# Kernel optimization log

Measured on AMD Instinct MI355X. Metric: run time of the kernel, lower is better.

Reference implementation:

```python
import jax, jax.numpy as jnp
import numpy as np

B, P, H, D = 32, 512, 512, 512

def setup_inputs() -> dict:
    key = jax.random.key(0)
    k1, k2, k3, k4 = jax.random.split(key, 4)
    px = jax.random.normal(k1, (B, P, D), dtype=jnp.float32)
    hx = jax.random.normal(k2, (B, H, D), dtype=jnp.float32)
    p_mask = jax.random.randint(k3, (B, P), 0, 2) == 1  # True = padded
    h_mask = jax.random.randint(k4, (B, H), 0, 2) == 1
    return {"px": px, "hx": hx, "p_mask": p_mask, "h_mask": h_mask}

def reference(px, hx, p_mask, h_mask):
    # shared (unscaled) score matrix: [B, P, H]
    e = jnp.einsum('bpd,bhd->bph', px, hx)
    neg_inf = jnp.float32(-jnp.inf)
    h_bias = jnp.where(h_mask, neg_inf, 0.0).astype(e.dtype)  # [B, H]
    p_bias = jnp.where(p_mask, neg_inf, 0.0).astype(e.dtype)  # [B, P]
    # softmax over hypothesis axis -> attend px to hx
    weight_b = jax.nn.softmax(e + h_bias[:, None, :], axis=2)  # [B, P, H]
    px_hat = jnp.einsum('bph,bhd->bpd', weight_b, hx)
    # softmax over premise axis -> attend hx to px
    weight_a = jax.nn.softmax(e + p_bias[:, :, None], axis=1)  # [B, P, H]
    hx_hat = jnp.einsum('bph,bpd->bhd', weight_a, px)
    m_p = jnp.concatenate([px, px_hat, px - px_hat, px * px_hat], axis=-1)
    m_h = jnp.concatenate([hx, hx_hat, hx - hx_hat, hx * hx_hat], axis=-1)
    return (m_p, m_h)
```

## Files before the change

### kernel.cpp

```cpp
#include <hip/hip_runtime.h>
#include <math.h>

#define NB 32
#define NN 512
#define ROWC 2048ull

typedef __attribute__((ext_vector_type(8))) short bf16x8;
typedef __attribute__((ext_vector_type(4))) float f32x4;

__device__ __forceinline__ unsigned int fbits(float f) {
  union { float f; unsigned int u; } v; v.f = f; return v.u;
}
__device__ __forceinline__ float bcast(unsigned int u) {
  union { unsigned int u; float f; } v; v.u = u; return v.f;
}
__device__ __forceinline__ unsigned int bf16_rne(float f) {
  unsigned int b = fbits(f);
  return (b + 0x7FFFu + ((b >> 16) & 1u)) >> 16;
}

__device__ __forceinline__ int frag_byte(int blk, int lane, int khalf) {
  int base = ((((khalf << 3) + blk) << 6) + lane) << 4;
  int swz = (blk ^ (lane >> 4) ^ (khalf << 2)) & 7;
  return base ^ (swz << 4);
}

__global__ __launch_bounds__(512) void gemm_e_stats(
    const float* __restrict__ px, const float* __restrict__ hx,
    const int* __restrict__ p_mask, const int* __restrict__ h_mask,
    float* __restrict__ e,
    float* __restrict__ rpm, float* __restrict__ rps,
    float* __restrict__ cpm, float* __restrict__ cps) {
  __shared__ union {
    struct { char Ah[16384]; char Al[16384]; char Bh[16384]; char Bl[16384]; } s;
    float ep[64][132];
  } u;
  __shared__ int pmk[128], hmk[128];
  __shared__ float st_m[2][128], st_s[2][128], sc_m[4][128], sc_s[4][128];
  const int b = blockIdx.z;
  const float* A = px + (size_t)b * NN * NN;
  const float* B = hx + (size_t)b * NN * NN;
  float* C = e + (size_t)b * NN * NN;
  const int row0 = blockIdx.y * 128, col0 = blockIdx.x * 128;
  const int t = threadIdx.x;
  const int l = t & 63, w = t >> 6;
  const int wr = w >> 1, wc = w & 1;
  const int g = l >> 4, li = l & 15;

  if (t < 128) pmk[t] = p_mask[(size_t)b * NN + row0 + t];
  else if (t < 256) hmk[t - 128] = h_mask[(size_t)b * NN + col0 + (t - 128)];

  f32x4 acc[2][4];
#pragma unroll
  for (int i = 0; i < 2; ++i)
#pragma unroll
    for (int j = 0; j < 4; ++j)
#pragma unroll
      for (int r = 0; r < 4; ++r) acc[i][j][r] = 0.f;

  for (int k0 = 0; k0 < NN; k0 += 64) {
#pragma unroll
    for (int i = 0; i < 4; ++i) {
      int idx = i * 512 + t;
      int r = idx >> 4, c4 = idx & 15, k = c4 << 2;
      int khalf = k >> 5, k8 = (k >> 3) & 3, j = k & 7;
      int byte = frag_byte(r >> 4, (r & 15) + (k8 << 4), khalf) + (j << 1);
      float4 f = *(const float4*)&A[(size_t)(row0 + r) * NN + k0 + k];
      unsigned int b0 = fbits(f.x), b1 = fbits(f.y), b2 = fbits(f.z), b3 = fbits(f.w);
      unsigned int h01 = (b0 >> 16) | (b1 & 0xFFFF0000u);
      unsigned int h23 = (b2 >> 16) | (b3 & 0xFFFF0000u);
      float r0 = f.x - bcast(b0 & 0xFFFF0000u);
      float r1 = f.y - bcast(b1 & 0xFFFF0000u);
      float r2 = f.z - bcast(b2 & 0xFFFF0000u);
      float r3 = f.w - bcast(b3 & 0xFFFF0000u);
      unsigned int l01 = (fbits(r0) >> 16) | (fbits(r1) & 0xFFFF0000u);
      unsigned int l23 = (fbits(r2) >> 16) | (fbits(r3) & 0xFFFF0000u);
      *(uint2*)&u.s.Ah[byte] = make_uint2(h01, h23);
      *(uint2*)&u.s.Al[byte] = make_uint2(l01, l23);
    }
#pragma unroll
    for (int i = 0; i < 4; ++i) {
      int idx = i * 512 + t;
      int r = idx >> 4, c4 = idx & 15, k = c4 << 2;
      int khalf = k >> 5, k8 = (k >> 3) & 3, j = k & 7;
      int byte = frag_byte(r >> 4, (r & 15) + (k8 << 4), khalf) + (j << 1);
      float4 f = *(const float4*)&B[(size_t)(col0 + r) * NN + k0 + k];
      unsigned int b0 = fbits(f.x), b1 = fbits(f.y), b2 = fbits(f.z), b3 = fbits(f.w);
      unsigned int h01 = (b0 >> 16) | (b1 & 0xFFFF0000u);
      unsigned int h23 = (b2 >> 16) | (b3 & 0xFFFF0000u);
      float r0 = f.x - bcast(b0 & 0xFFFF0000u);
      float r1 = f.y - bcast(b1 & 0xFFFF0000u);
      float r2 = f.z - bcast(b2 & 0xFFFF0000u);
      float r3 = f.w - bcast(b3 & 0xFFFF0000u);
      unsigned int l01 = (fbits(r0) >> 16) | (fbits(r1) & 0xFFFF0000u);
      unsigned int l23 = (fbits(r2) >> 16) | (fbits(r3) & 0xFFFF0000u);
      *(uint2*)&u.s.Bh[byte] = make_uint2(h01, h23);
      *(uint2*)&u.s.Bl[byte] = make_uint2(l01, l23);
    }
    __syncthreads();

#pragma unroll
    for (int kh = 0; kh < 2; ++kh) {
      bf16x8 ah[2], al[2];
#pragma unroll
      for (int i = 0; i < 2; ++i) {
        int ab = frag_byte(wr * 2 + i, l, kh);
        ah[i] = *(const bf16x8*)&u.s.Ah[ab];
        al[i] = *(const bf16x8*)&u.s.Al[ab];
      }
#pragma unroll
      for (int j = 0; j < 4; ++j) {
        int bb = frag_byte(wc * 4 + j, l, kh);
        bf16x8 bh = *(const bf16x8*)&u.s.Bh[bb];
        bf16x8 bl = *(const bf16x8*)&u.s.Bl[bb];
#pragma unroll
        for (int i = 0; i < 2; ++i) {
          acc[i][j] = __builtin_amdgcn_mfma_f32_16x16x32_bf16(ah[i], bh, acc[i][j], 0, 0, 0);
          acc[i][j] = __builtin_amdgcn_mfma_f32_16x16x32_bf16(ah[i], bl, acc[i][j], 0, 0, 0);
          acc[i][j] = __builtin_amdgcn_mfma_f32_16x16x32_bf16(al[i], bh, acc[i][j], 0, 0, 0);
        }
      }
    }
    __syncthreads();
  }

#pragma unroll
  for (int i = 0; i < 2; ++i)
#pragma unroll
    for (int r = 0; r < 4; ++r) {
      float v[4];
      float m = -INFINITY;
#pragma unroll
      for (int j = 0; j < 4; ++j) {
        v[j] = hmk[wc * 64 + j * 16 + li] ? -INFINITY : acc[i][j][r];
        m = fmaxf(m, v[j]);
      }
#pragma unroll
      for (int o = 1; o < 16; o <<= 1) m = fmaxf(m, __shfl_xor(m, o));
      float s = 0.f;
#pragma unroll
      for (int j = 0; j < 4; ++j) s += (v[j] == -INFINITY) ? 0.f : __expf(v[j] - m);
#pragma unroll
      for (int o = 1; o < 16; o <<= 1) s += __shfl_xor(s, o);
      if (li == 0) {
        st_m[wc][wr * 32 + i * 16 + g * 4 + r] = m;
        st_s[wc][wr * 32 + i * 16 + g * 4 + r] = s;
      }
    }

#pragma unroll
  for (int j = 0; j < 4; ++j) {
    float v[8];
    float m = -INFINITY;
#pragma unroll
    for (int i = 0; i < 2; ++i)
#pragma unroll
      for (int r = 0; r < 4; ++r) {
        float x = pmk[wr * 32 + i * 16 + g * 4 + r] ? -INFINITY : acc[i][j][r];
        v[i * 4 + r] = x;
        m = fmaxf(m, x);
      }
    m = fmaxf(m, __shfl_xor(m, 16));
    m = fmaxf(m, __shfl_xor(m, 32));
    float s = 0.f;
#pragma unroll
    for (int q = 0; q < 8; ++q) s += (v[q] == -INFINITY) ? 0.f : __expf(v[q] - m);
    s += __shfl_xor(s, 16);
    s += __shfl_xor(s, 32);
    if (g == 0) {
      sc_m[wr][wc * 64 + j * 16 + li] = m;
      sc_s[wr][wc * 64 + j * 16 + li] = s;
    }
  }
  __syncthreads();

  if (t < 128) {
    float m0 = st_m[0][t], m1 = st_m[1][t];
    float s0 = st_s[0][t], s1 = st_s[1][t];
    float m = fmaxf(m0, m1);
    float s = 0.f;
    if (s0 > 0.f) s += s0 * __expf(m0 - m);
    if (s1 > 0.f) s += s1 * __expf(m1 - m);
    rpm[((size_t)b * 4 + blockIdx.x) * NN + row0 + t] = m;
    rps[((size_t)b * 4 + blockIdx.x) * NN + row0 + t] = s;
  } else if (t < 256) {
    int c = t - 128;
    float m = sc_m[0][c];
#pragma unroll
    for (int q = 1; q < 4; ++q) m = fmaxf(m, sc_m[q][c]);
    float s = 0.f;
#pragma unroll
    for (int q = 0; q < 4; ++q)
      if (sc_s[q][c] > 0.f) s += sc_s[q][c] * __expf(sc_m[q][c] - m);
    cpm[((size_t)b * 4 + blockIdx.y) * NN + col0 + c] = m;
    cps[((size_t)b * 4 + blockIdx.y) * NN + col0 + c] = s;
  }

#pragma unroll
  for (int pass = 0; pass < 2; ++pass) {
    __syncthreads();
    if ((wr >> 1) == pass) {
#pragma unroll
      for (int i = 0; i < 2; ++i)
#pragma unroll
        for (int j = 0; j < 4; ++j)
#pragma unroll
          for (int r = 0; r < 4; ++r)
            u.ep[(wr & 1) * 32 + i * 16 + g * 4 + r][wc * 64 + j * 16 + li] = acc[i][j][r];
    }
    __syncthreads();
#pragma unroll
    for (int i = 0; i < 4; ++i) {
      int idx = i * 512 + t;
      int r = idx >> 5, c4 = idx & 31;
      int grow = row0 + pass * 64 + r;
      float4 v = *(const float4*)&u.ep[r][c4 * 4];
      *(float4*)&C[(size_t)grow * NN + col0 + c4 * 4] = v;
    }
  }
}

__global__ __launch_bounds__(512) void merge_stats(
    const float* __restrict__ rpm, const float* __restrict__ rps,
    const float* __restrict__ cpm, const float* __restrict__ cps,
    float* __restrict__ rmax, float* __restrict__ rinv,
    float* __restrict__ cmax, float* __restrict__ cinv) {
  const int b = blockIdx.x;
  const int t = threadIdx.x;
  const float* pm = blockIdx.y == 0 ? rpm : cpm;
  const float* ps = blockIdx.y == 0 ? rps : cps;
  float* fm = blockIdx.y == 0 ? rmax : cmax;
  float* fi = blockIdx.y == 0 ? rinv : cinv;
  float mj[4], sj[4];
  float m = -INFINITY;
#pragma unroll
  for (int j = 0; j < 4; ++j) {
    mj[j] = pm[((size_t)b * 4 + j) * NN + t];
    sj[j] = ps[((size_t)b * 4 + j) * NN + t];
    m = fmaxf(m, mj[j]);
  }
  float s = 0.f;
#pragma unroll
  for (int j = 0; j < 4; ++j)
    if (sj[j] > 0.f) s += sj[j] * __expf(mj[j] - m);
  fm[(size_t)b * NN + t] = m;
  fi[(size_t)b * NN + t] = 1.0f / s;
}

__global__ __launch_bounds__(256) void gemm_wp(
    const float* __restrict__ E, const float* __restrict__ hxg,
    const float* __restrict__ pxg, const int* __restrict__ h_mask,
    const float* __restrict__ rmax, const float* __restrict__ rinv,
    float* __restrict__ outg) {
  __shared__ union {
    struct { char A[16384]; char B[16384]; } s;
    float ep[64][132];
  } u;
  const int b = blockIdx.z;
  const float* Eb = E + (size_t)b * NN * NN;
  const float* B = hxg + (size_t)b * NN * NN;
  const float* X = pxg + (size_t)b * NN * NN;
  const int* hm = h_mask + (size_t)b * NN;
  const float* rmx = rmax + (size_t)b * NN;
  const float* rin = rinv + (size_t)b * NN;
  float* out = outg + (size_t)b * NN * ROWC;
  const int row0 = blockIdx.y * 128, col0 = blockIdx.x * 128;
  const int t = threadIdx.x;
  const int l = t & 63, w = t >> 6;
  const int wr = w >> 1, wc = w & 1;

  float rmv[8];
#pragma unroll
  for (int i = 0; i < 8; ++i) rmv[i] = rmx[row0 + ((i * 256 + t) >> 4)];

  f32x4 acc[4][4];
#pragma unroll
  for (int i = 0; i < 4; ++i)
#pragma unroll
    for (int j = 0; j < 4; ++j)
#pragma unroll
      for (int r = 0; r < 4; ++r) acc[i][j][r] = 0.f;

  for (int k0 = 0; k0 < NN; k0 += 64) {
#pragma unroll
    for (int i = 0; i < 8; ++i) {
      int idx = i * 256 + t;
      int r = idx >> 4, c4 = idx & 15, k = c4 << 2;
      float4 f = *(const float4*)&Eb[(size_t)(row0 + r) * NN + k0 + k];
      int4 m4 = *(const int4*)&hm[k0 + k];
      float w0 = m4.x ? 0.f : __expf(f.x - rmv[i]);
      float w1 = m4.y ? 0.f : __expf(f.y - rmv[i]);
      float w2 = m4.z ? 0.f : __expf(f.z - rmv[i]);
      float w3 = m4.w ? 0.f : __expf(f.w - rmv[i]);
      unsigned int p01 = bf16_rne(w0) | (bf16_rne(w1) << 16);
      unsigned int p23 = bf16_rne(w2) | (bf16_rne(w3) << 16);
      int khalf = k >> 5, k8 = (k >> 3) & 3, j = k & 7;
      int byte = frag_byte(r >> 4, (r & 15) + (k8 << 4), khalf) + (j << 1);
      *(uint2*)&u.s.A[byte] = make_uint2(p01, p23);
    }
#pragma unroll
    for (int i = 0; i < 4; ++i) {
      int idx = i * 256 + t;
      int kp = idx >> 5, nq = idx & 31;
      int k = kp << 1, n = nq << 2;
      const float* p0 = &B[(size_t)(k0 + k) * NN + col0 + n];
      float4 f0 = *(const float4*)p0;
      float4 f1 = *(const float4*)(p0 + NN);
      int khalf = k >> 5, k8 = (k >> 3) & 3, j = k & 7;
      float fa0[4] = {f0.x, f0.y, f0.z, f0.w};
      float fa1[4] = {f1.x, f1.y, f1.z, f1.w};
#pragma unroll
      for (int c = 0; c < 4; ++c) {
        unsigned int pk = bf16_rne(fa0[c]) | (bf16_rne(fa1[c]) << 16);
        int nn2 = n + c;
        int byte = frag_byte(nn2 >> 4, (nn2 & 15) + (k8 << 4), khalf) + (j << 1);
        *(unsigned int*)&u.s.B[byte] = pk;
      }
    }
    __syncthreads();
#pragma unroll
    for (int kh = 0; kh < 2; ++kh) {
      bf16x8 av[4], bv[4];
#pragma unroll
      for (int i = 0; i < 4; ++i) {
        av[i] = *(const bf16x8*)&u.s.A[frag_byte(wr * 4 + i, l, kh)];
        bv[i] = *(const bf16x8*)&u.s.B[frag_byte(wc * 4 + i, l, kh)];
      }
#pragma unroll
      for (int i = 0; i < 4; ++i)
#pragma unroll
        for (int j = 0; j < 4; ++j)
          acc[i][j] = __builtin_amdgcn_mfma_f32_16x16x32_bf16(av[i], bv[j], acc[i][j], 0, 0, 0);
    }
    __syncthreads();
  }

  const int g = l >> 4, li = l & 15;
#pragma unroll
  for (int pass = 0; pass < 2; ++pass) {
    if (wr == pass) {
#pragma unroll
      for (int i = 0; i < 4; ++i)
#pragma unroll
        for (int j = 0; j < 4; ++j)
#pragma unroll
          for (int r = 0; r < 4; ++r)
            u.ep[i * 16 + g * 4 + r][wc * 64 + j * 16 + li] = acc[i][j][r];
    }
    __syncthreads();
#pragma unroll
    for (int i = 0; i < 8; ++i) {
      int idx = i * 256 + t;
      int r = idx >> 5, c4 = idx & 31;
      int grow = row0 + pass * 64 + r;
      float ri = rin[grow];
      float4 ph = *(const float4*)&u.ep[r][c4 * 4];
      ph.x *= ri; ph.y *= ri; ph.z *= ri; ph.w *= ri;
      float4 xv = *(const float4*)&X[(size_t)grow * NN + col0 + c4 * 4];
      size_t base = (size_t)grow * ROWC + col0 + c4 * 4;
      *(float4*)&out[base] = xv;
      *(float4*)&out[base + 512] = ph;
      float4 df = {xv.x - ph.x, xv.y - ph.y, xv.z - ph.z, xv.w - ph.w};
      *(float4*)&out[base + 1024] = df;
      float4 pr = {xv.x * ph.x, xv.y * ph.y, xv.z * ph.z, xv.w * ph.w};
      *(float4*)&out[base + 1536] = pr;
    }
    __syncthreads();
  }
}

__global__ __launch_bounds__(256) void gemm_wh(
    const float* __restrict__ E, const float* __restrict__ pxg,
    const float* __restrict__ hxg, const int* __restrict__ p_mask,
    const float* __restrict__ cmax, const float* __restrict__ cinv,
    float* __restrict__ outg) {
  __shared__ union {
    struct { char A[16384]; char B[16384]; } s;
    float ep[64][132];
  } u;
  const int b = blockIdx.z;
  const float* Eb = E + (size_t)b * NN * NN;
  const float* B = pxg + (size_t)b * NN * NN;
  const float* X = hxg + (size_t)b * NN * NN;
  const int* pmsk = p_mask + (size_t)b * NN;
  const float* cmx = cmax + (size_t)b * NN;
  const float* cin = cinv + (size_t)b * NN;
  float* out = outg + (size_t)b * NN * ROWC;
  const int row0 = blockIdx.y * 128, col0 = blockIdx.x * 128;
  const int t = threadIdx.x;
  const int l = t & 63, w = t >> 6;
  const int wr = w >> 1, wc = w & 1;

  float4 cmv[4];
#pragma unroll
  for (int i = 0; i < 4; ++i) {
    int idx = i * 256 + t;
    int n = (idx & 31) << 2;
    cmv[i] = *(const float4*)&cmx[row0 + n];
  }

  f32x4 acc[4][4];
#pragma unroll
  for (int i = 0; i < 4; ++i)
#pragma unroll
    for (int j = 0; j < 4; ++j)
#pragma unroll
      for (int r = 0; r < 4; ++r) acc[i][j][r] = 0.f;

  for (int k0 = 0; k0 < NN; k0 += 64) {
#pragma unroll
    for (int i = 0; i < 4; ++i) {
      int idx = i * 256 + t;
      int kp = idx >> 5, nq = idx & 31;
      int k = kp << 1, n = nq << 2;
      const float* p0 = &Eb[(size_t)(k0 + k) * NN + row0 + n];
      float4 f0 = *(const float4*)p0;
      float4 f1 = *(const float4*)(p0 + NN);
      int pm0 = pmsk[k0 + k], pm1 = pmsk[k0 + k + 1];
      float fa0[4] = {f0.x, f0.y, f0.z, f0.w};
      float fa1[4] = {f1.x, f1.y, f1.z, f1.w};
      float cma[4] = {cmv[i].x, cmv[i].y, cmv[i].z, cmv[i].w};
      int khalf = k >> 5, k8 = (k >> 3) & 3, j = k & 7;
#pragma unroll
      for (int c = 0; c < 4; ++c) {
        float w0 = pm0 ? 0.f : __expf(fa0[c] - cma[c]);
        float w1 = pm1 ? 0.f : __expf(fa1[c] - cma[c]);
        unsigned int pk = bf16_rne(w0) | (bf16_rne(w1) << 16);
        int nn2 = n + c;
        int byte = frag_byte(nn2 >> 4, (nn2 & 15) + (k8 << 4), khalf) + (j << 1);
        *(unsigned int*)&u.s.A[byte] = pk;
      }
    }
#pragma unroll
    for (int i = 0; i < 4; ++i) {
      int idx = i * 256 + t;
      int kp = idx >> 5, nq = idx & 31;
      int k = kp << 1, n = nq << 2;
      const float* p0 = &B[(size_t)(k0 + k) * NN + col0 + n];
      float4 f0 = *(const float4*)p0;
      float4 f1 = *(const float4*)(p0 + NN);
      int khalf = k >> 5, k8 = (k >> 3) & 3, j = k & 7;
      float fa0[4] = {f0.x, f0.y, f0.z, f0.w};
      float fa1[4] = {f1.x, f1.y, f1.z, f1.w};
#pragma unroll
      for (int c = 0; c < 4; ++c) {
        unsigned int pk = bf16_rne(fa0[c]) | (bf16_rne(fa1[c]) << 16);
        int nn2 = n + c;
        int byte = frag_byte(nn2 >> 4, (nn2 & 15) + (k8 << 4), khalf) + (j << 1);
        *(unsigned int*)&u.s.B[byte] = pk;
      }
    }
    __syncthreads();
#pragma unroll
    for (int kh = 0; kh < 2; ++kh) {
      bf16x8 av[4], bv[4];
#pragma unroll
      for (int i = 0; i < 4; ++i) {
        av[i] = *(const bf16x8*)&u.s.A[frag_byte(wr * 4 + i, l, kh)];
        bv[i] = *(const bf16x8*)&u.s.B[frag_byte(wc * 4 + i, l, kh)];
      }
#pragma unroll
      for (int i = 0; i < 4; ++i)
#pragma unroll
        for (int j = 0; j < 4; ++j)
          acc[i][j] = __builtin_amdgcn_mfma_f32_16x16x32_bf16(av[i], bv[j], acc[i][j], 0, 0, 0);
    }
    __syncthreads();
  }

  const int g = l >> 4, li = l & 15;
#pragma unroll
  for (int pass = 0; pass < 2; ++pass) {
    if (wr == pass) {
#pragma unroll
      for (int i = 0; i < 4; ++i)
#pragma unroll
        for (int j = 0; j < 4; ++j)
#pragma unroll
          for (int r = 0; r < 4; ++r)
            u.ep[i * 16 + g * 4 + r][wc * 64 + j * 16 + li] = acc[i][j][r];
    }
    __syncthreads();
#pragma unroll
    for (int i = 0; i < 8; ++i) {
      int idx = i * 256 + t;
      int r = idx >> 5, c4 = idx & 31;
      int grow = row0 + pass * 64 + r;
      float ci = cin[grow];
      float4 hh = *(const float4*)&u.ep[r][c4 * 4];
      hh.x *= ci; hh.y *= ci; hh.z *= ci; hh.w *= ci;
      float4 xv = *(const float4*)&X[(size_t)grow * NN + col0 + c4 * 4];
      size_t base = (size_t)grow * ROWC + col0 + c4 * 4;
      *(float4*)&out[base] = xv;
      *(float4*)&out[base + 512] = hh;
      float4 df = {xv.x - hh.x, xv.y - hh.y, xv.z - hh.z, xv.w - hh.w};
      *(float4*)&out[base + 1024] = df;
      float4 pr = {xv.x * hh.x, xv.y * hh.y, xv.z * hh.z, xv.w * hh.w};
      *(float4*)&out[base + 1536] = pr;
    }
    __syncthreads();
  }
}

extern "C" void kernel_launch(void* const* d_in, const int* in_sizes, int n_in,
                              void* d_out, int out_size, void* d_ws, size_t ws_size,
                              hipStream_t stream) {
  const float* px = (const float*)d_in[0];
  const float* hx = (const float*)d_in[1];
  const int* p_mask = (const int*)d_in[2];
  const int* h_mask = (const int*)d_in[3];
  float* out = (float*)d_out;

  float* E = (float*)d_ws;
  float* rpm = E + (size_t)NB * NN * NN;
  float* rps = rpm + (size_t)NB * 4 * NN;
  float* cpm = rps + (size_t)NB * 4 * NN;
  float* cps = cpm + (size_t)NB * 4 * NN;
  float* rmaxv = cps + (size_t)NB * 4 * NN;
  float* rinvv = rmaxv + (size_t)NB * NN;
  float* cmaxv = rinvv + (size_t)NB * NN;
  float* cinvv = cmaxv + (size_t)NB * NN;

  dim3 gg(4, 4, NB);
  gemm_e_stats<<<gg, dim3(512), 0, stream>>>(px, hx, p_mask, h_mask, E, rpm, rps, cpm, cps);
  merge_stats<<<dim3(NB, 2), dim3(512), 0, stream>>>(rpm, rps, cpm, cps,
                                                     rmaxv, rinvv, cmaxv, cinvv);
  gemm_wp<<<gg, dim3(256), 0, stream>>>(E, hx, px, h_mask, rmaxv, rinvv, out);
  gemm_wh<<<gg, dim3(256), 0, stream>>>(E, px, hx, p_mask, cmaxv, cinvv,
                                        out + (size_t)NB * NN * ROWC);
}
```

Measured before the change: 250.0 us.

## Prefetch next K tile into registers and simplify swizzled LDS layout in E-GEMM

Global loads for the next 64-wide K slice of px/hx are issued into registers right after the barrier, so they overlap with the MFMA work on the current slice. The LDS staging layout changes to a row-major XOR-swizzled layout (ebyte) with cheaper address math for both stores and fragment reads. Mask values are loaded into registers instead of shared memory, and the softmax-stat scratch arrays now share the union with the tile buffers, which lowers LDS footprint. Holding 8 extra float4 values per thread raises register pressure and could reduce occupancy.

After: 208.9 us. 1.2x faster.

```diff
diff --git a/kernel.cpp b/kernel.cpp
--- a/kernel.cpp
+++ b/kernel.cpp
@@ -23,6 +23,10 @@
   int base = ((((khalf << 3) + blk) << 6) + lane) << 4;
   int swz = (blk ^ (lane >> 4) ^ (khalf << 2)) & 7;
   return base ^ (swz << 4);
+}
+
+__device__ __forceinline__ int ebyte(int row, int unit) {
+  return row * 128 + ((unit ^ (row & 7)) << 4);
 }
 
 __global__ __launch_bounds__(512) void gemm_e_stats(
@@ -33,10 +37,10 @@
     float* __restrict__ cpm, float* __restrict__ cps) {
   __shared__ union {
     struct { char Ah[16384]; char Al[16384]; char Bh[16384]; char Bl[16384]; } s;
+    struct { float st_m[2][128]; float st_s[2][128];
+             float sc_m[4][128]; float sc_s[4][128]; } x;
     float ep[64][132];
   } u;
-  __shared__ int pmk[128], hmk[128];
-  __shared__ float st_m[2][128], st_s[2][128], sc_m[4][128], sc_s[4][128];
   const int b = blockIdx.z;
   const float* A = px + (size_t)b * NN * NN;
   const float* B = hx + (size_t)b * NN * NN;
@@ -47,9 +51,6 @@
   const int wr = w >> 1, wc = w & 1;
   const int g = l >> 4, li = l & 15;
 
-  if (t < 128) pmk[t] = p_mask[(size_t)b * NN + row0 + t];
-  else if (t < 256) hmk[t - 128] = h_mask[(size_t)b * NN + col0 + (t - 128)];
-
   f32x4 acc[2][4];
 #pragma unroll
   for (int i = 0; i < 2; ++i)
@@ -58,14 +59,23 @@
 #pragma unroll
       for (int r = 0; r < 4; ++r) acc[i][j][r] = 0.f;
 
+  const int sr = t >> 4, su = t & 15;
+  const int sbyte0 = ((su >> 1) << 4);
+  const int shalf = (su & 1) * 8;
+
+  float4 fa[4], fb[4];
+#pragma unroll
+  for (int i = 0; i < 4; ++i) {
+    fa[i] = *(const float4*)&A[(size_t)(row0 + sr + 32 * i) * NN + su * 4];
+    fb[i] = *(const float4*)&B[(size_t)(col0 + sr + 32 * i) * NN + su * 4];
+  }
+
   for (int k0 = 0; k0 < NN; k0 += 64) {
 #pragma unroll
     for (int i = 0; i < 4; ++i) {
-      int idx = i * 512 + t;
-      int r = idx >> 4, c4 = idx & 15, k = c4 << 2;
-      int khalf = k >> 5, k8 = (k >> 3) & 3, j = k & 7;
-      int byte = frag_byte(r >> 4, (r & 15) + (k8 << 4), khalf) + (j << 1);
-      float4 f = *(const float4*)&A[(size_t)(row0 + r) * NN + k0 + k];
+      int r = sr + 32 * i;
+      int byte = r * 128 + ((((su >> 1) ^ (r & 7)) << 4)) + shalf;
+      float4 f = fa[i];
       unsigned int b0 = fbits(f.x), b1 = fbits(f.y), b2 = fbits(f.z), b3 = fbits(f.w);
       unsigned int h01 = (b0 >> 16) | (b1 & 0xFFFF0000u);
       unsigned int h23 = (b2 >> 16) | (b3 & 0xFFFF0000u);
@@ -77,40 +87,43 @@
       unsigned int l23 = (fbits(r2) >> 16) | (fbits(r3) & 0xFFFF0000u);
       *(uint2*)&u.s.Ah[byte] = make_uint2(h01, h23);
       *(uint2*)&u.s.Al[byte] = make_uint2(l01, l23);
-    }
-#pragma unroll
-    for (int i = 0; i < 4; ++i) {
-      int idx = i * 512 + t;
-      int r = idx >> 4, c4 = idx & 15, k = c4 << 2;
-      int khalf = k >> 5, k8 = (k >> 3) & 3, j = k & 7;
-      int byte = frag_byte(r >> 4, (r & 15) + (k8 << 4), khalf) + (j << 1);
-      float4 f = *(const float4*)&B[(size_t)(col0 + r) * NN + k0 + k];
-      unsigned int b0 = fbits(f.x), b1 = fbits(f.y), b2 = fbits(f.z), b3 = fbits(f.w);
-      unsigned int h01 = (b0 >> 16) | (b1 & 0xFFFF0000u);
-      unsigned int h23 = (b2 >> 16) | (b3 & 0xFFFF0000u);
-      float r0 = f.x - bcast(b0 & 0xFFFF0000u);
-      float r1 = f.y - bcast(b1 & 0xFFFF0000u);
-      float r2 = f.z - bcast(b2 & 0xFFFF0000u);
-      float r3 = f.w - bcast(b3 & 0xFFFF0000u);
-      unsigned int l01 = (fbits(r0) >> 16) | (fbits(r1) & 0xFFFF0000u);
-      unsigned int l23 = (fbits(r2) >> 16) | (fbits(r3) & 0xFFFF0000u);
+      f = fb[i];
+      b0 = fbits(f.x); b1 = fbits(f.y); b2 = fbits(f.z); b3 = fbits(f.w);
+      h01 = (b0 >> 16) | (b1 & 0xFFFF0000u);
+      h23 = (b2 >> 16) | (b3 & 0xFFFF0000u);
+      r0 = f.x - bcast(b0 & 0xFFFF0000u);
+      r1 = f.y - bcast(b1 & 0xFFFF0000u);
+      r2 = f.z - bcast(b2 & 0xFFFF0000u);
+      r3 = f.w - bcast(b3 & 0xFFFF0000u);
+      l01 = (fbits(r0) >> 16) | (fbits(r1) & 0xFFFF0000u);
+      l23 = (fbits(r2) >> 16) | (fbits(r3) & 0xFFFF0000u);
       *(uint2*)&u.s.Bh[byte] = make_uint2(h01, h23);
       *(uint2*)&u.s.Bl[byte] = make_uint2(l01, l23);
     }
     __syncthreads();
 
+    if (k0 + 64 < NN) {
+#pragma unroll
+      for (int i = 0; i < 4; ++i) {
+        fa[i] = *(const float4*)&A[(size_t)(row0 + sr + 32 * i) * NN + k0 + 64 + su * 4];
+        fb[i] = *(const float4*)&B[(size_t)(col0 + sr + 32 * i) * NN + k0 + 64 + su * 4];
+      }
+    }
+
 #pragma unroll
     for (int kh = 0; kh < 2; ++kh) {
       bf16x8 ah[2], al[2];
 #pragma unroll
       for (int i = 0; i < 2; ++i) {
-        int ab = frag_byte(wr * 2 + i, l, kh);
+        int row = wr * 32 + i * 16 + li;
+        int ab = ebyte(row, kh * 4 + g);
         ah[i] = *(const bf16x8*)&u.s.Ah[ab];
         al[i] = *(const bf16x8*)&u.s.Al[ab];
       }
 #pragma unroll
       for (int j = 0; j < 4; ++j) {
-        int bb = frag_byte(wc * 4 + j, l, kh);
+        int col = wc * 64 + j * 16 + li;
+        int bb = ebyte(col, kh * 4 + g);
         bf16x8 bh = *(const bf16x8*)&u.s.Bh[bb];
         bf16x8 bl = *(const bf16x8*)&u.s.Bl[bb];
 #pragma unroll
@@ -124,6 +137,16 @@
     __syncthreads();
   }
 
+  int hmr[4], pmr[2][4];
+#pragma unroll
+  for (int j = 0; j < 4; ++j)
+    hmr[j] = h_mask[(size_t)b * NN + col0 + wc * 64 + j * 16 + li];
+#pragma unroll
+  for (int i = 0; i < 2; ++i)
+#pragma unroll
+    for (int r = 0; r < 4; ++r)
+      pmr[i][r] = p_mask[(size_t)b * NN + row0 + wr * 32 + i * 16 + g * 4 + r];
+
 #pragma unroll
   for (int i = 0; i < 2; ++i)
 #pragma unroll
@@ -132,7 +155,7 @@
       float m = -INFINITY;
 #pragma unroll
       for (int j = 0; j < 4; ++j) {
-        v[j] = hmk[wc * 64 + j * 16 + li] ? -INFINITY : acc[i][j][r];
+        v[j] = hmr[j] ? -INFINITY : acc[i][j][r];
         m = fmaxf(m, v[j]);
       }
 #pragma unroll
@@ -143,8 +166,8 @@
 #pragma unroll
       for (int o = 1; o < 16; o <<= 1) s += __shfl_xor(s, o);
       if (li == 0) {
-        st_m[wc][wr * 32 + i * 16 + g * 4 + r] = m;
-        st_s[wc][wr * 32 + i * 16 + g * 4 + r] = s;
+        u.x.st_m[wc][wr * 32 + i * 16 + g * 4 + r] = m;
+        u.x.st_s[wc][wr * 32 + i * 16 + g * 4 + r] = s;
       }
     }
 
@@ -156,7 +179,7 @@
     for (int i = 0; i < 2; ++i)
 #pragma unroll
       for (int r = 0; r < 4; ++r) {
-        float x = pmk[wr * 32 + i * 16 + g * 4 + r] ? -INFINITY : acc[i][j][r];
+        float x = pmr[i][r] ? -INFINITY : acc[i][j][r];
         v[i * 4 + r] = x;
         m = fmaxf(m, x);
       }
@@ -168,15 +191,15 @@
     s += __shfl_xor(s, 16);
     s += __shfl_xor(s, 32);
     if (g == 0) {
-      sc_m[wr][wc * 64 + j * 16 + li] = m;
-      sc_s[wr][wc * 64 + j * 16 + li] = s;
+      u.x.sc_m[wr][wc * 64 + j * 16 + li] = m;
+      u.x.sc_s[wr][wc * 64 + j * 16 + li] = s;
     }
   }
   __syncthreads();
 
   if (t < 128) {
-    float m0 = st_m[0][t], m1 = st_m[1][t];
-    float s0 = st_s[0][t], s1 = st_s[1][t];
+    float m0 = u.x.st_m[0][t], m1 = u.x.st_m[1][t];
+    float s0 = u.x.st_s[0][t], s1 = u.x.st_s[1][t];
     float m = fmaxf(m0, m1);
     float s = 0.f;
     if (s0 > 0.f) s += s0 * __expf(m0 - m);
@@ -185,13 +208,13 @@
     rps[((size_t)b * 4 + blockIdx.x) * NN + row0 + t] = s;
   } else if (t < 256) {
     int c = t - 128;
-    float m = sc_m[0][c];
-#pragma unroll
-    for (int q = 1; q < 4; ++q) m = fmaxf(m, sc_m[q][c]);
+    float m = u.x.sc_m[0][c];
+#pragma unroll
+    for (int q = 1; q < 4; ++q) m = fmaxf(m, u.x.sc_m[q][c]);
     float s = 0.f;
 #pragma unroll
     for (int q = 0; q < 4; ++q)
-      if (sc_s[q][c] > 0.f) s += sc_s[q][c] * __expf(sc_m[q][c] - m);
+      if (u.x.sc_s[q][c] > 0.f) s += u.x.sc_s[q][c] * __expf(u.x.sc_m[q][c] - m);
     cpm[((size_t)b * 4 + blockIdx.y) * NN + col0 + c] = m;
     cps[((size_t)b * 4 + blockIdx.y) * NN + col0 + c] = s;
   }
```

## Split softmax stats out of score GEMM into separate row/column reduction kernels

Applied to the files above, without the earlier changes.

The score GEMM no longer computes per-tile softmax max/sum partials. It now runs 256 threads per block, each wave owning a 64x64 sub-tile, with a K step of 32 and half the shared staging. Row and column max/sum statistics are computed by two new kernels that re-read the full E matrix from global memory, replacing the partial-stats merge. This shrinks the GEMM epilogue and its register and LDS pressure, but adds an extra full pass over E (32x512x512 floats), and the column kernel reads with a strided pattern.

Result: no change. 247.0 us (-1.2%).

```diff
diff --git a/kernel.cpp b/kernel.cpp
--- a/kernel.cpp
+++ b/kernel.cpp
@@ -25,18 +25,19 @@
   return base ^ (swz << 4);
 }
 
-__global__ __launch_bounds__(512) void gemm_e_stats(
+__device__ __forceinline__ int frag32(int blk, int lane) {
+  int base = (blk << 10) + (lane << 4);
+  int swz = (blk ^ (lane >> 4)) & 7;
+  return base ^ (swz << 4);
+}
+
+__global__ __launch_bounds__(256) void gemm_e(
     const float* __restrict__ px, const float* __restrict__ hx,
-    const int* __restrict__ p_mask, const int* __restrict__ h_mask,
-    float* __restrict__ e,
-    float* __restrict__ rpm, float* __restrict__ rps,
-    float* __restrict__ cpm, float* __restrict__ cps) {
+    float* __restrict__ e) {
   __shared__ union {
-    struct { char Ah[16384]; char Al[16384]; char Bh[16384]; char Bl[16384]; } s;
+    struct { char Ah[8192]; char Al[8192]; char Bh[8192]; char Bl[8192]; } s;
     float ep[64][132];
   } u;
-  __shared__ int pmk[128], hmk[128];
-  __shared__ float st_m[2][128], st_s[2][128], sc_m[4][128], sc_s[4][128];
   const int b = blockIdx.z;
   const float* A = px + (size_t)b * NN * NN;
   const float* B = hx + (size_t)b * NN * NN;
@@ -45,26 +46,21 @@
   const int t = threadIdx.x;
   const int l = t & 63, w = t >> 6;
   const int wr = w >> 1, wc = w & 1;
-  const int g = l >> 4, li = l & 15;
-
-  if (t < 128) pmk[t] = p_mask[(size_t)b * NN + row0 + t];
-  else if (t < 256) hmk[t - 128] = h_mask[(size_t)b * NN + col0 + (t - 128)];
-
-  f32x4 acc[2][4];
-#pragma unroll
-  for (int i = 0; i < 2; ++i)
+
+  f32x4 acc[4][4];
+#pragma unroll
+  for (int i = 0; i < 4; ++i)
 #pragma unroll
     for (int j = 0; j < 4; ++j)
 #pragma unroll
       for (int r = 0; r < 4; ++r) acc[i][j][r] = 0.f;
 
-  for (int k0 = 0; k0 < NN; k0 += 64) {
-#pragma unroll
-    for (int i = 0; i < 4; ++i) {
-      int idx = i * 512 + t;
-      int r = idx >> 4, c4 = idx & 15, k = c4 << 2;
-      int khalf = k >> 5, k8 = (k >> 3) & 3, j = k & 7;
-      int byte = frag_byte(r >> 4, (r & 15) + (k8 << 4), khalf) + (j << 1);
+  for (int k0 = 0; k0 < NN; k0 += 32) {
+#pragma unroll
+    for (int i = 0; i < 4; ++i) {
+      int idx = i * 256 + t;
+      int r = idx >> 3, c4 = idx & 7, k = c4 << 2;
+      int byte = frag32(r >> 4, (r & 15) + ((c4 >> 1) << 4)) + (c4 & 1) * 8;
       float4 f = *(const float4*)&A[(size_t)(row0 + r) * NN + k0 + k];
       unsigned int b0 = fbits(f.x), b1 = fbits(f.y), b2 = fbits(f.z), b3 = fbits(f.w);
       unsigned int h01 = (b0 >> 16) | (b1 & 0xFFFF0000u);
@@ -80,10 +76,9 @@
     }
 #pragma unroll
     for (int i = 0; i < 4; ++i) {
-      int idx = i * 512 + t;
-      int r = idx >> 4, c4 = idx & 15, k = c4 << 2;
-      int khalf = k >> 5, k8 = (k >> 3) & 3, j = k & 7;
-      int byte = frag_byte(r >> 4, (r & 15) + (k8 << 4), khalf) + (j << 1);
+      int idx = i * 256 + t;
+      int r = idx >> 3, c4 = idx & 7, k = c4 << 2;
+      int byte = frag32(r >> 4, (r & 15) + ((c4 >> 1) << 4)) + (c4 & 1) * 8;
       float4 f = *(const float4*)&B[(size_t)(col0 + r) * NN + k0 + k];
       unsigned int b0 = fbits(f.x), b1 = fbits(f.y), b2 = fbits(f.z), b3 = fbits(f.w);
       unsigned int h01 = (b0 >> 16) | (b1 & 0xFFFF0000u);
@@ -99,152 +94,128 @@
     }
     __syncthreads();
 
-#pragma unroll
-    for (int kh = 0; kh < 2; ++kh) {
-      bf16x8 ah[2], al[2];
-#pragma unroll
-      for (int i = 0; i < 2; ++i) {
-        int ab = frag_byte(wr * 2 + i, l, kh);
-        ah[i] = *(const bf16x8*)&u.s.Ah[ab];
-        al[i] = *(const bf16x8*)&u.s.Al[ab];
-      }
-#pragma unroll
-      for (int j = 0; j < 4; ++j) {
-        int bb = frag_byte(wc * 4 + j, l, kh);
-        bf16x8 bh = *(const bf16x8*)&u.s.Bh[bb];
-        bf16x8 bl = *(const bf16x8*)&u.s.Bl[bb];
-#pragma unroll
-        for (int i = 0; i < 2; ++i) {
-          acc[i][j] = __builtin_amdgcn_mfma_f32_16x16x32_bf16(ah[i], bh, acc[i][j], 0, 0, 0);
-          acc[i][j] = __builtin_amdgcn_mfma_f32_16x16x32_bf16(ah[i], bl, acc[i][j], 0, 0, 0);
-          acc[i][j] = __builtin_amdgcn_mfma_f32_16x16x32_bf16(al[i], bh, acc[i][j], 0, 0, 0);
-        }
-      }
-    }
-    __syncthreads();
-  }
-
-#pragma unroll
-  for (int i = 0; i < 2; ++i)
-#pragma unroll
-    for (int r = 0; r < 4; ++r) {
-      float v[4];
-      float m = -INFINITY;
-#pragma unroll
-      for (int j = 0; j < 4; ++j) {
-        v[j] = hmk[wc * 64 + j * 16 + li] ? -INFINITY : acc[i][j][r];
-        m = fmaxf(m, v[j]);
-      }
-#pragma unroll
-      for (int o = 1; o < 16; o <<= 1) m = fmaxf(m, __shfl_xor(m, o));
-      float s = 0.f;
-#pragma unroll
-      for (int j = 0; j < 4; ++j) s += (v[j] == -INFINITY) ? 0.f : __expf(v[j] - m);
-#pragma unroll
-      for (int o = 1; o < 16; o <<= 1) s += __shfl_xor(s, o);
-      if (li == 0) {
-        st_m[wc][wr * 32 + i * 16 + g * 4 + r] = m;
-        st_s[wc][wr * 32 + i * 16 + g * 4 + r] = s;
-      }
-    }
-
-#pragma unroll
-  for (int j = 0; j < 4; ++j) {
-    float v[8];
-    float m = -INFINITY;
-#pragma unroll
-    for (int i = 0; i < 2; ++i)
-#pragma unroll
-      for (int r = 0; r < 4; ++r) {
-        float x = pmk[wr * 32 + i * 16 + g * 4 + r] ? -INFINITY : acc[i][j][r];
-        v[i * 4 + r] = x;
-        m = fmaxf(m, x);
-      }
-    m = fmaxf(m, __shfl_xor(m, 16));
-    m = fmaxf(m, __shfl_xor(m, 32));
-    float s = 0.f;
-#pragma unroll
-    for (int q = 0; q < 8; ++q) s += (v[q] == -INFINITY) ? 0.f : __expf(v[q] - m);
-    s += __shfl_xor(s, 16);
-    s += __shfl_xor(s, 32);
-    if (g == 0) {
-      sc_m[wr][wc * 64 + j * 16 + li] = m;
-      sc_s[wr][wc * 64 + j * 16 + li] = s;
-    }
-  }
-  __syncthreads();
-
-  if (t < 128) {
-    float m0 = st_m[0][t], m1 = st_m[1][t];
-    float s0 = st_s[0][t], s1 = st_s[1][t];
-    float m = fmaxf(m0, m1);
-    float s = 0.f;
-    if (s0 > 0.f) s += s0 * __expf(m0 - m);
-    if (s1 > 0.f) s += s1 * __expf(m1 - m);
-    rpm[((size_t)b * 4 + blockIdx.x) * NN + row0 + t] = m;
-    rps[((size_t)b * 4 + blockIdx.x) * NN + row0 + t] = s;
-  } else if (t < 256) {
-    int c = t - 128;
-    float m = sc_m[0][c];
-#pragma unroll
-    for (int q = 1; q < 4; ++q) m = fmaxf(m, sc_m[q][c]);
-    float s = 0.f;
-#pragma unroll
-    for (int q = 0; q < 4; ++q)
-      if (sc_s[q][c] > 0.f) s += sc_s[q][c] * __expf(sc_m[q][c] - m);
-    cpm[((size_t)b * 4 + blockIdx.y) * NN + col0 + c] = m;
-    cps[((size_t)b * 4 + blockIdx.y) * NN + col0 + c] = s;
-  }
-
+    bf16x8 ah[4], al[4];
+#pragma unroll
+    for (int i = 0; i < 4; ++i) {
+      int ab = frag32(wr * 4 + i, l);
+      ah[i] = *(const bf16x8*)&u.s.Ah[ab];
+      al[i] = *(const bf16x8*)&u.s.Al[ab];
+    }
+#pragma unroll
+    for (int j = 0; j < 4; ++j) {
+      int bb = frag32(wc * 4 + j, l);
+      bf16x8 bh = *(const bf16x8*)&u.s.Bh[bb];
+      bf16x8 bl = *(const bf16x8*)&u.s.Bl[bb];
+#pragma unroll
+      for (int i = 0; i < 4; ++i) {
+        acc[i][j] = __builtin_amdgcn_mfma_f32_16x16x32_bf16(al[i], bh, acc[i][j], 0, 0, 0);
+        acc[i][j] = __builtin_amdgcn_mfma_f32_16x16x32_bf16(ah[i], bl, acc[i][j], 0, 0, 0);
+        acc[i][j] = __builtin_amdgcn_mfma_f32_16x16x32_bf16(ah[i], bh, acc[i][j], 0, 0, 0);
+      }
+    }
+    __syncthreads();
+  }
+
+  const int g = l >> 4, li = l & 15;
 #pragma unroll
   for (int pass = 0; pass < 2; ++pass) {
-    __syncthreads();
-    if ((wr >> 1) == pass) {
-#pragma unroll
-      for (int i = 0; i < 2; ++i)
+    if (wr == pass) {
+#pragma unroll
+      for (int i = 0; i < 4; ++i)
 #pragma unroll
         for (int j = 0; j < 4; ++j)
 #pragma unroll
           for (int r = 0; r < 4; ++r)
-            u.ep[(wr & 1) * 32 + i * 16 + g * 4 + r][wc * 64 + j * 16 + li] = acc[i][j][r];
-    }
-    __syncthreads();
-#pragma unroll
-    for (int i = 0; i < 4; ++i) {
-      int idx = i * 512 + t;
+            u.ep[i * 16 + g * 4 + r][wc * 64 + j * 16 + li] = acc[i][j][r];
+    }
+    __syncthreads();
+#pragma unroll
+    for (int i = 0; i < 8; ++i) {
+      int idx = i * 256 + t;
       int r = idx >> 5, c4 = idx & 31;
       int grow = row0 + pass * 64 + r;
       float4 v = *(const float4*)&u.ep[r][c4 * 4];
       *(float4*)&C[(size_t)grow * NN + col0 + c4 * 4] = v;
     }
-  }
-}
-
-__global__ __launch_bounds__(512) void merge_stats(
-    const float* __restrict__ rpm, const float* __restrict__ rps,
-    const float* __restrict__ cpm, const float* __restrict__ cps,
-    float* __restrict__ rmax, float* __restrict__ rinv,
+    __syncthreads();
+  }
+}
+
+__global__ __launch_bounds__(512) void row_stats(
+    const float* __restrict__ e, const int* __restrict__ h_mask,
+    float* __restrict__ rmax, float* __restrict__ rinv) {
+  const int b = blockIdx.x, oct = blockIdx.y;
+  __shared__ int hm[512];
+  const int t = threadIdx.x;
+  if (t < 128) *(int4*)&hm[t * 4] = *(const int4*)&h_mask[(size_t)b * NN + t * 4];
+  __syncthreads();
+  const int row = oct * 64 + (t >> 3), seg = t & 7;
+  const float* er = e + (size_t)b * NN * NN + (size_t)row * NN + seg * 64;
+  float m = -INFINITY, s = 0.f;
+#pragma unroll
+  for (int i = 0; i < 16; ++i) {
+    float4 f = *(const float4*)&er[i * 4];
+    int4 msk = *(const int4*)&hm[seg * 64 + i * 4];
+    float vv[4] = {f.x, f.y, f.z, f.w};
+    int mk[4] = {msk.x, msk.y, msk.z, msk.w};
+#pragma unroll
+    for (int c = 0; c < 4; ++c) {
+      if (!mk[c]) {
+        float mn = fmaxf(m, vv[c]);
+        s = s * __expf(m - mn) + __expf(vv[c] - mn);
+        m = mn;
+      }
+    }
+  }
+#pragma unroll
+  for (int o = 1; o < 8; o <<= 1) {
+    float m2 = __shfl_xor(m, o), s2 = __shfl_xor(s, o);
+    float mn = fmaxf(m, m2);
+    float sn = 0.f;
+    if (s > 0.f) sn += s * __expf(m - mn);
+    if (s2 > 0.f) sn += s2 * __expf(m2 - mn);
+    m = mn; s = sn;
+  }
+  if (seg == 0) {
+    rmax[(size_t)b * NN + row] = m;
+    rinv[(size_t)b * NN + row] = 1.0f / s;
+  }
+}
+
+__global__ __launch_bounds__(512) void col_stats(
+    const float* __restrict__ e, const int* __restrict__ p_mask,
     float* __restrict__ cmax, float* __restrict__ cinv) {
-  const int b = blockIdx.x;
+  const int b = blockIdx.x, oct = blockIdx.y;
+  __shared__ int pm[512];
   const int t = threadIdx.x;
-  const float* pm = blockIdx.y == 0 ? rpm : cpm;
-  const float* ps = blockIdx.y == 0 ? rps : cps;
-  float* fm = blockIdx.y == 0 ? rmax : cmax;
-  float* fi = blockIdx.y == 0 ? rinv : cinv;
-  float mj[4], sj[4];
-  float m = -INFINITY;
-#pragma unroll
-  for (int j = 0; j < 4; ++j) {
-    mj[j] = pm[((size_t)b * 4 + j) * NN + t];
-    sj[j] = ps[((size_t)b * 4 + j) * NN + t];
-    m = fmaxf(m, mj[j]);
-  }
-  float s = 0.f;
-#pragma unroll
-  for (int j = 0; j < 4; ++j)
-    if (sj[j] > 0.f) s += sj[j] * __expf(mj[j] - m);
-  fm[(size_t)b * NN + t] = m;
-  fi[(size_t)b * NN + t] = 1.0f / s;
+  if (t < 128) *(int4*)&pm[t * 4] = *(const int4*)&p_mask[(size_t)b * NN + t * 4];
+  __syncthreads();
+  const int col = oct * 64 + (t >> 3), seg = t & 7;
+  const float* ec = e + (size_t)b * NN * NN + col;
+  float m = -INFINITY, s = 0.f;
+#pragma unroll 8
+  for (int i = 0; i < 64; ++i) {
+    int p = seg * 64 + i;
+    if (!pm[p]) {
+      float v = ec[(size_t)p * NN];
+      float mn = fmaxf(m, v);
+      s = s * __expf(m - mn) + __expf(v - mn);
+      m = mn;
+    }
+  }
+#pragma unroll
+  for (int o = 1; o < 8; o <<= 1) {
+    float m2 = __shfl_xor(m, o), s2 = __shfl_xor(s, o);
+    float mn = fmaxf(m, m2);
+    float sn = 0.f;
+    if (s > 0.f) sn += s * __expf(m - mn);
+    if (s2 > 0.f) sn += s2 * __expf(m2 - mn);
+    m = mn; s = sn;
+  }
+  if (seg == 0) {
+    cmax[(size_t)b * NN + col] = m;
+    cinv[(size_t)b * NN + col] = 1.0f / s;
+  }
 }
 
 __global__ __launch_bounds__(256) void gemm_wp(
@@ -512,19 +483,15 @@
   float* out = (float*)d_out;
 
   float* E = (float*)d_ws;
-  float* rpm = E + (size_t)NB * NN * NN;
-  float* rps = rpm + (size_t)NB * 4 * NN;
-  float* cpm = rps + (size_t)NB * 4 * NN;
-  float* cps = cpm + (size_t)NB * 4 * NN;
-  float* rmaxv = cps + (size_t)NB * 4 * NN;
+  float* rmaxv = E + (size_t)NB * NN * NN;
   float* rinvv = rmaxv + (size_t)NB * NN;
   float* cmaxv = rinvv + (size_t)NB * NN;
   float* cinvv = cmaxv + (size_t)NB * NN;
 
   dim3 gg(4, 4, NB);
-  gemm_e_stats<<<gg, dim3(512), 0, stream>>>(px, hx, p_mask, h_mask, E, rpm, rps, cpm, cps);
-  merge_stats<<<dim3(NB, 2), dim3(512), 0, stream>>>(rpm, rps, cpm, cps,
-                                                     rmaxv, rinvv, cmaxv, cinvv);
+  gemm_e<<<gg, dim3(256), 0, stream>>>(px, hx, E);
+  row_stats<<<dim3(NB, 8), dim3(512), 0, stream>>>(E, h_mask, rmaxv, rinvv);
+  col_stats<<<dim3(NB, 8), dim3(512), 0, stream>>>(E, p_mask, cmaxv, cinvv);
   gemm_wp<<<gg, dim3(256), 0, stream>>>(E, hx, px, h_mask, rmaxv, rinvv, out);
   gemm_wh<<<gg, dim3(256), 0, stream>>>(E, px, hx, p_mask, cmaxv, cinvv,
                                         out + (size_t)NB * NN * ROWC);
```
